# Kernel optimization log

Measured on AMD Instinct MI355X. Metric: run time of the kernel, lower is better.

## Reference

```python
import jax, jax.numpy as jnp
import numpy as np

N = 50000          # nodes (multiple of p+e=8)
E = 400000         # edges (avg degree 8)
H, C = 4, 128      # heads, per-head channels
IN = 5             # input node feature dim
HID = 512          # mlp hidden dim
P, EV = 4, 4       # pursuers / evaders per graph
NEG_SLOPE = 0.2    # GATConv leaky_relu slope

# static team index: nodes with idx % (P+EV) < P  (team='pursuer')
_idx = np.arange(N)
TEAM_IDX = jnp.asarray(_idx[_idx % (P + EV) < P])  # [N/2]


def setup_inputs() -> dict:
    key = jax.random.key(0)
    ks = jax.random.split(key, 16)
    s = 0.1
    return {
        "x": jax.random.normal(ks[0], (N, IN), jnp.float32),
        "edge_index": jax.random.randint(ks[1], (2, E), 0, N, jnp.int64),
        "edge_attr": jax.random.normal(ks[2], (E, 2), jnp.float32),
        # GATConv params
        "W": jax.random.normal(ks[3], (H * C, IN), jnp.float32) * s,
        "att_src": jax.random.normal(ks[4], (H, C), jnp.float32) * s,
        "att_dst": jax.random.normal(ks[5], (H, C), jnp.float32) * s,
        "bias": jnp.zeros((H * C,), jnp.float32),
        # MLP head params
        "W1": jax.random.normal(ks[6], (HID, H * C), jnp.float32) * s,
        "b1": jnp.zeros((HID,), jnp.float32),
        "W2": jax.random.normal(ks[7], (HID, HID), jnp.float32) * s,
        "b2": jnp.zeros((HID,), jnp.float32),
        "W3": jax.random.normal(ks[8], (2, HID), jnp.float32) * s,
        "b3": jnp.zeros((2,), jnp.float32),
    }


def _gat_max(x, src, dst, W, att_src, att_dst, bias):
    # linear transform: [N, H, C]
    h = (x @ W.T).reshape(N, H, C)
    a_src = jnp.einsum("nhc,hc->nh", h, att_src)  # [N, H]
    a_dst = jnp.einsum("nhc,hc->nh", h, att_dst)  # [N, H]
    # per-edge attention logits, leaky relu
    alpha = jax.nn.leaky_relu(a_src[src] + a_dst[dst], NEG_SLOPE)  # [Et, H]
    # segment softmax over incoming edges of each dst node
    amax = jax.ops.segment_max(alpha, dst, num_segments=N)  # [N, H]
    ex = jnp.exp(alpha - amax[dst])
    den = jax.ops.segment_sum(ex, dst, num_segments=N)      # [N, H]
    attn = ex / den[dst]                                     # [Et, H]
    # alpha-weighted messages, scatter-MAX aggregation (aggr='max')
    msg = h[src] * attn[:, :, None]                          # [Et, H, C]
    out = jax.ops.segment_max(msg, dst, num_segments=N)     # [N, H, C]
    return out.reshape(N, H * C) + bias


def reference(x, edge_index, edge_attr, W, att_src, att_dst, bias,
              W1, b1, W2, b2, W3, b3):
    # PyG GATConv default add_self_loops=True; edge_attr ignored (edge_dim=None)
    loops = jnp.arange(N, dtype=edge_index.dtype)
    src = jnp.concatenate([edge_index[0], loops])
    dst = jnp.concatenate([edge_index[1], loops])
    emb = _gat_max(x, src, dst, W, att_src, att_dst, bias)  # [N, 512]
    h = emb[TEAM_IDX]                                        # [N/2, 512]
    h = jax.nn.relu(h @ W1.T + b1)
    h = jax.nn.relu(h @ W2.T + b2)
    return jnp.tanh(h @ W3.T + b3)                           # [N/2, 2]
```

## Files before the change

### kernel.cpp

```cpp
#include <hip/hip_runtime.h>
#include <hip/hip_bf16.h>
#include <math.h>

#define N_NODES 50000
#define N_EDGES 400000
#define HEADS   4
#define HC      512
#define IN_DIM  5
#define M_SEL   25000
#define NEG_SLOPE 0.2f

typedef __attribute__((ext_vector_type(8))) short bf16x8;
typedef __attribute__((ext_vector_type(4))) float f32x4;

__device__ inline unsigned short f2bf(float f) {
    union { float f; unsigned u; } v; v.f = f;
    unsigned r = v.u + 0x7FFF + ((v.u >> 16) & 1);
    return (unsigned short)(r >> 16);
}
__device__ inline float bf2f(unsigned short b) {
    union { unsigned u; float f; } v; v.u = ((unsigned)b) << 16;
    return v.f;
}

#define GLOAD_LDS16(g, l)                                                  \
    __builtin_amdgcn_global_load_lds(                                      \
        (const __attribute__((address_space(1))) unsigned int*)(g),        \
        (__attribute__((address_space(3))) unsigned int*)(l), 16, 0, 0)

__global__ void k_init(const float* __restrict__ W1, const float* __restrict__ W2,
                       unsigned short* __restrict__ W1b, unsigned short* __restrict__ W2b,
                       float* __restrict__ part, int* __restrict__ deg) {
    int i = blockIdx.x * 256 + threadIdx.x;
    const float* src = (i < 65536) ? W1 : W2;
    unsigned short* dst = (i < 65536) ? W1b : W2b;
    int j = i & 65535;
    float4 v = ((const float4*)src)[j];
    ushort4 o;
    o.x = f2bf(v.x); o.y = f2bf(v.y); o.z = f2bf(v.z); o.w = f2bf(v.w);
    ((ushort4*)dst)[j] = o;
    if (i < 2 * M_SEL) part[i] = 0.f;
    if (i < N_NODES) deg[i] = 1;
}

#define TR_NPW 8
#define TR_BLKS 1563

__global__ __launch_bounds__(256) void k_transform_hist(
        const float* __restrict__ x, const float* __restrict__ W,
        const float* __restrict__ att_src, const float* __restrict__ att_dst,
        unsigned short* __restrict__ h, float* __restrict__ a_src,
        float* __restrict__ a_dst, const int* __restrict__ ei,
        int* __restrict__ deg) {
    if (blockIdx.x >= TR_BLKS) {
        int e = (blockIdx.x - TR_BLKS) * 256 + threadIdx.x;
        if (e < N_EDGES) atomicAdd(&deg[ei[N_EDGES + e]], 1);
        return;
    }
    int wave = threadIdx.x >> 6, lane = threadIdx.x & 63;
    int c0 = lane * 8;

    float wreg[40];
    const float4* wp = (const float4*)(W + c0 * IN_DIM);
#pragma unroll
    for (int i = 0; i < 10; i++) ((float4*)wreg)[i] = wp[i];
    float sas[8], sad[8];
    *(float4*)&sas[0] = *(const float4*)(att_src + c0);
    *(float4*)&sas[4] = *(const float4*)(att_src + c0 + 4);
    *(float4*)&sad[0] = *(const float4*)(att_dst + c0);
    *(float4*)&sad[4] = *(const float4*)(att_dst + c0 + 4);

    int n0 = (blockIdx.x * 4 + wave) * TR_NPW;
#pragma unroll
    for (int t = 0; t < TR_NPW; t++) {
        int n = n0 + t;
        if (n >= N_NODES) return;
        float xv[IN_DIM];
#pragma unroll
        for (int i = 0; i < IN_DIM; i++) xv[i] = x[n * IN_DIM + i];

        float ps = 0.f, pd = 0.f;
        bf16x8 hv8;
#pragma unroll
        for (int j = 0; j < 8; j++) {
            float acc = 0.f;
#pragma unroll
            for (int i = 0; i < IN_DIM; i++) acc += xv[i] * wreg[j * IN_DIM + i];
            hv8[j] = (short)f2bf(acc);
            ps += acc * sas[j];
            pd += acc * sad[j];
        }
        *(bf16x8*)(h + (size_t)n * HC + c0) = hv8;

#pragma unroll
        for (int off = 8; off >= 1; off >>= 1) {
            ps += __shfl_xor(ps, off);
            pd += __shfl_xor(pd, off);
        }
        if ((lane & 15) == 0) {
            int head = lane >> 4;
            a_src[n * HEADS + head] = ps;
            a_dst[n * HEADS + head] = pd;
        }
    }
}

#define NSCAN_BLK 196

__global__ void k_scan1(const int* __restrict__ deg, int* __restrict__ excl,
                        int* __restrict__ bsum) {
    __shared__ int s[256];
    int i = blockIdx.x * 256 + threadIdx.x;
    int v = (i < N_NODES) ? deg[i] : 0;
    s[threadIdx.x] = v;
    __syncthreads();
    for (int off = 1; off < 256; off <<= 1) {
        int t = (threadIdx.x >= off) ? s[threadIdx.x - off] : 0;
        __syncthreads();
        s[threadIdx.x] += t;
        __syncthreads();
    }
    if (i < N_NODES) excl[i] = s[threadIdx.x] - v;
    if (threadIdx.x == 255) bsum[blockIdx.x] = s[255];
}

__global__ void k_scan3fill(const int* __restrict__ excl, const int* __restrict__ bsum,
                            int* __restrict__ offs, int* __restrict__ curs,
                            int* __restrict__ csr) {
    __shared__ int part[256];
    int tid = threadIdx.x;
    part[tid] = (tid < NSCAN_BLK) ? bsum[tid] : 0;
    __syncthreads();
    for (int off = 1; off < 256; off <<= 1) {
        int t = (tid >= off) ? part[tid - off] : 0;
        __syncthreads();
        part[tid] += t;
        __syncthreads();
    }
    int blockoff = (blockIdx.x == 0) ? 0 : part[blockIdx.x - 1];
    int i = blockIdx.x * 256 + tid;
    if (i < N_NODES) {
        int o = excl[i] + blockoff;
        offs[i] = o;
        csr[o] = i;
        curs[i] = o + 1;
    }
}

__global__ void k_fill_edges(const int* __restrict__ ei, int* __restrict__ cursor,
                             int* __restrict__ csr) {
    int e = blockIdx.x * 256 + threadIdx.x;
    if (e < N_EDGES) {
        int d = ei[N_EDGES + e];
        int pos = atomicAdd(&cursor[d], 1);
        csr[pos] = ei[e];
    }
}

__global__ __launch_bounds__(256, 4) void k_aggregate(
        const unsigned short* __restrict__ h, const float* __restrict__ a_src,
        const float* __restrict__ a_dst, const int* __restrict__ csr,
        const int* __restrict__ offs, const int* __restrict__ deg,
        const float* __restrict__ bias, unsigned short* __restrict__ emb_sel) {
    int wave = threadIdx.x >> 6, lane = threadIdx.x & 63;
    int w = blockIdx.x * 4 + wave;
    int n = ((w >> 2) << 3) + (w & 3);

    int base = offs[n];
    int dn = deg[n];
    int head = lane >> 4, egrp = lane & 15;
    int c0 = lane * 8;

    float acc[8];
#pragma unroll
    for (int j = 0; j < 8; j++) acc[j] = -INFINITY;

    if (dn <= 16) {
        int slot = (egrp < dn) ? egrp : (dn - 1);
        int s_e = csr[base + slot];
        float adn = a_dst[n * HEADS + head];
        float araw = a_src[s_e * HEADS + head];
        float tl = araw + adn;
        tl = (tl > 0.f) ? tl : NEG_SLOPE * tl;
        if (egrp >= dn) tl = -INFINITY;

        bf16x8 v[16];
#pragma unroll
        for (int e = 0; e < 16; e++) {
            int s = __shfl(s_e, e);
            const unsigned short* ap = h + (size_t)s * HC + c0;
            asm volatile("global_load_dwordx4 %0, %1, off"
                         : "=v"(v[e]) : "v"(ap) : "memory");
        }

        float m = tl;
#pragma unroll
        for (int off = 8; off >= 1; off >>= 1) m = fmaxf(m, __shfl_xor(m, off));
        float ex = (egrp < dn) ? __expf(tl - m) : 0.f;
        float den = ex;
#pragma unroll
        for (int off = 8; off >= 1; off >>= 1) den += __shfl_xor(den, off);
        float attn = ex / den;

#pragma unroll
        for (int e = 0; e < 16; e++) {
            asm volatile("s_waitcnt vmcnt(%1)" : "+v"(v[e]) : "i"(15 - e));
            int ei = (e < dn) ? e : (dn - 1);
            float a = __shfl(attn, (head << 4) | ei);
#pragma unroll
            for (int j = 0; j < 8; j++)
                acc[j] = fmaxf(acc[j], bf2f((unsigned short)v[e][j]) * a);
        }
    } else {
        float adn = a_dst[n * HEADS + head];
        float m = -INFINITY;
        for (int e0 = 0; e0 < dn; e0 += 16) {
            int e = e0 + egrp;
            if (e < dn) {
                int s = csr[base + e];
                float t = a_src[s * HEADS + head] + adn;
                t = (t > 0.f) ? t : NEG_SLOPE * t;
                m = fmaxf(m, t);
            }
        }
#pragma unroll
        for (int off = 8; off >= 1; off >>= 1) m = fmaxf(m, __shfl_xor(m, off));
        float den = 0.f;
        for (int e0 = 0; e0 < dn; e0 += 16) {
            int e = e0 + egrp;
            if (e < dn) {
                int s = csr[base + e];
                float t = a_src[s * HEADS + head] + adn;
                t = (t > 0.f) ? t : NEG_SLOPE * t;
                den += __expf(t - m);
            }
        }
#pragma unroll
        for (int off = 8; off >= 1; off >>= 1) den += __shfl_xor(den, off);
        float invden = 1.0f / den;
        for (int e = 0; e < dn; e++) {
            int s = csr[base + e];
            float t = a_src[s * HEADS + head] + adn;
            t = (t > 0.f) ? t : NEG_SLOPE * t;
            float attn = __expf(t - m) * invden;
            bf16x8 hv = *(const bf16x8*)(h + (size_t)s * HC + c0);
#pragma unroll
            for (int j = 0; j < 8; j++)
                acc[j] = fmaxf(acc[j], bf2f((unsigned short)hv[j]) * attn);
        }
    }

    bf16x8 ov;
#pragma unroll
    for (int j = 0; j < 8; j++) ov[j] = (short)f2bf(acc[j] + bias[c0 + j]);
    *(bf16x8*)(emb_sel + (size_t)w * HC + c0) = ov;
}

template <int MODE>
__global__ __launch_bounds__(256, 4) void k_gemm(const unsigned short* __restrict__ A, int M,
                                                 const unsigned short* __restrict__ Wt,
                                                 const float* __restrict__ bias,
                                                 unsigned short* __restrict__ C,
                                                 const float* __restrict__ W3,
                                                 float* __restrict__ part) {
    __shared__ unsigned short As[128 * 64];
    __shared__ unsigned short Bs[128 * 64];
    int tid = threadIdx.x;
    int m0 = blockIdx.y * 128;
    int o0 = blockIdx.x * 128;
    int wv = tid >> 6, lane = tid & 63;
    int wm = wv >> 1, wn = wv & 1;

    f32x4 acc[4][4];
#pragma unroll
    for (int i = 0; i < 4; i++)
#pragma unroll
        for (int j = 0; j < 4; j++) acc[i][j] = (f32x4){0.f, 0.f, 0.f, 0.f};

    for (int k0 = 0; k0 < HC; k0 += 64) {
#pragma unroll
        for (int c = 0; c < 4; c++) {
            int off = wv * 4096 + c * 1024 + lane * 16;
            int row = off >> 7, col = (off & 127) >> 1;
            GLOAD_LDS16(A + (size_t)(m0 + row) * HC + k0 + col,
                        (char*)As + off);
            GLOAD_LDS16(Wt + (size_t)(o0 + row) * HC + k0 + col,
                        (char*)Bs + off);
        }
        __syncthreads();

#pragma unroll
        for (int kk = 0; kk < 2; kk++) {
            int kb = kk * 32 + (lane >> 4) * 8;
            bf16x8 af[4], bfr[4];
#pragma unroll
            for (int mi = 0; mi < 4; mi++)
                af[mi] = *(const bf16x8*)(&As[(wm * 64 + mi * 16 + (lane & 15)) * 64 + kb]);
#pragma unroll
            for (int ni = 0; ni < 4; ni++)
                bfr[ni] = *(const bf16x8*)(&Bs[(wn * 64 + ni * 16 + (lane & 15)) * 64 + kb]);
#pragma unroll
            for (int mi = 0; mi < 4; mi++)
#pragma unroll
                for (int ni = 0; ni < 4; ni++)
                    acc[mi][ni] = __builtin_amdgcn_mfma_f32_16x16x32_bf16(
                        af[mi], bfr[ni], acc[mi][ni], 0, 0, 0);
        }
        __syncthreads();
    }

    if (MODE == 0) {
#pragma unroll
        for (int ni = 0; ni < 4; ni++) {
            int ncol = o0 + wn * 64 + ni * 16 + (lane & 15);
            float bv = bias[ncol];
#pragma unroll
            for (int mi = 0; mi < 4; mi++) {
                int mbase = m0 + wm * 64 + mi * 16 + (lane >> 4) * 4;
#pragma unroll
                for (int r = 0; r < 4; r++) {
                    int m = mbase + r;
                    if (m < M) {
                        float v = fmaxf(acc[mi][ni][r] + bv, 0.f);
                        C[(size_t)m * HC + ncol] = f2bf(v);
                    }
                }
            }
        }
    } else {
        float p0[4][4], p1[4][4];
#pragma unroll
        for (int mi = 0; mi < 4; mi++)
#pragma unroll
            for (int r = 0; r < 4; r++) { p0[mi][r] = 0.f; p1[mi][r] = 0.f; }
#pragma unroll
        for (int ni = 0; ni < 4; ni++) {
            int ncol = o0 + wn * 64 + ni * 16 + (lane & 15);
            float bv = bias[ncol];
            float w0 = W3[ncol], w1 = W3[HC + ncol];
#pragma unroll
            for (int mi = 0; mi < 4; mi++)
#pragma unroll
                for (int r = 0; r < 4; r++) {
                    float v = fmaxf(acc[mi][ni][r] + bv, 0.f);
                    p0[mi][r] += v * w0;
                    p1[mi][r] += v * w1;
                }
        }
#pragma unroll
        for (int mi = 0; mi < 4; mi++)
#pragma unroll
            for (int r = 0; r < 4; r++) {
                float a0 = p0[mi][r], a1 = p1[mi][r];
#pragma unroll
                for (int off = 8; off >= 1; off >>= 1) {
                    a0 += __shfl_xor(a0, off);
                    a1 += __shfl_xor(a1, off);
                }
                int m = m0 + wm * 64 + mi * 16 + (lane >> 4) * 4 + r;
                if ((lane & 15) == 0 && m < M) {
                    atomicAdd(&part[m * 2 + 0], a0);
                    atomicAdd(&part[m * 2 + 1], a1);
                }
            }
    }
}

__global__ void k_tanh(const float* __restrict__ part, const float* __restrict__ b3,
                       float* __restrict__ out) {
    int i = blockIdx.x * 256 + threadIdx.x;
    if (i < 2 * M_SEL) out[i] = tanhf(part[i] + b3[i & 1]);
}

extern "C" void kernel_launch(void* const* d_in, const int* in_sizes, int n_in,
                              void* d_out, int out_size, void* d_ws, size_t ws_size,
                              hipStream_t stream) {
    const float* x       = (const float*)d_in[0];
    const int*   ei      = (const int*)d_in[1];
    const float* W       = (const float*)d_in[3];
    const float* att_src = (const float*)d_in[4];
    const float* att_dst = (const float*)d_in[5];
    const float* bias    = (const float*)d_in[6];
    const float* W1      = (const float*)d_in[7];
    const float* b1      = (const float*)d_in[8];
    const float* W2      = (const float*)d_in[9];
    const float* b2      = (const float*)d_in[10];
    const float* W3      = (const float*)d_in[11];
    const float* b3      = (const float*)d_in[12];
    float* out = (float*)d_out;

    char* ws = (char*)d_ws;
    unsigned short* h       = (unsigned short*)(ws);
    unsigned short* emb_sel = (unsigned short*)(ws + 51200000);
    unsigned short* h1      = (unsigned short*)(ws + 76800000);
    float* part  = (float*)(ws + 102400000);
    float* a_src = (float*)(ws + 102600000);
    float* a_dst = (float*)(ws + 103400000);
    int*   deg   = (int*)  (ws + 104200000);
    int*   offs  = (int*)  (ws + 104400000);
    int*   curs  = (int*)  (ws + 104600000);
    int*   excl  = (int*)  (ws + 104800000);
    int*   bsum  = (int*)  (ws + 105000000);
    int*   csr   = (int*)  (ws + 105001024);
    unsigned short* W1b = (unsigned short*)(ws + 106801024);
    unsigned short* W2b = (unsigned short*)(ws + 107325312);

    k_init<<<512, 256, 0, stream>>>(W1, W2, W1b, W2b, part, deg);
    k_transform_hist<<<TR_BLKS * 2, 256, 0, stream>>>(x, W, att_src, att_dst, h,
                                                      a_src, a_dst, ei, deg);
    k_scan1<<<NSCAN_BLK, 256, 0, stream>>>(deg, excl, bsum);
    k_scan3fill<<<NSCAN_BLK, 256, 0, stream>>>(excl, bsum, offs, curs, csr);
    k_fill_edges<<<(N_EDGES + 255) / 256, 256, 0, stream>>>(ei, curs, csr);
    k_aggregate<<<6250, 256, 0, stream>>>(h, a_src, a_dst, csr, offs, deg, bias, emb_sel);

    dim3 g(4, 196);
    k_gemm<0><<<g, 256, 0, stream>>>(emb_sel, M_SEL, W1b, b1, h1, nullptr, nullptr);
    k_gemm<1><<<g, 256, 0, stream>>>(h1, M_SEL, W2b, b2, nullptr, W3, part);
    k_tanh<<<196, 256, 0, stream>>>(part, b3, out);
}
```

Measured before the change: 180.7 us.

## Enlarge GEMM tile to 256x128 and simplify low-degree aggregation loads

The MLP GEMM now uses 256-row tiles where each wave owns 64 rows and all 128 output columns, with launch bounds lowered to 2 blocks per SM and half as many row blocks. This increases B-tile reuse per LDS load. The aggregate kernel drops the hand-issued 16-load inline asm prefetch with manual waitcnt in favour of a loop over actual degree, unrolled by 4. It also adds a bounds guard. Risks: GEMM register pressure doubles accumulators (possible lower occupancy), and aggregation loses the deep memory-level parallelism of 16 outstanding loads.

```diff
diff --git a/kernel.cpp b/kernel.cpp
--- a/kernel.cpp
+++ b/kernel.cpp
@@ -157,13 +157,13 @@
     }
 }
 
-__global__ __launch_bounds__(256, 4) void k_aggregate(
-        const unsigned short* __restrict__ h, const float* __restrict__ a_src,
-        const float* __restrict__ a_dst, const int* __restrict__ csr,
-        const int* __restrict__ offs, const int* __restrict__ deg,
-        const float* __restrict__ bias, unsigned short* __restrict__ emb_sel) {
+__global__ void k_aggregate(const unsigned short* __restrict__ h, const float* __restrict__ a_src,
+                            const float* __restrict__ a_dst, const int* __restrict__ csr,
+                            const int* __restrict__ offs, const int* __restrict__ deg,
+                            const float* __restrict__ bias, unsigned short* __restrict__ emb_sel) {
     int wave = threadIdx.x >> 6, lane = threadIdx.x & 63;
     int w = blockIdx.x * 4 + wave;
+    if (w >= M_SEL) return;
     int n = ((w >> 2) << 3) + (w & 3);
 
     int base = offs[n];
@@ -176,40 +176,49 @@
     for (int j = 0; j < 8; j++) acc[j] = -INFINITY;
 
     if (dn <= 16) {
-        int slot = (egrp < dn) ? egrp : (dn - 1);
-        int s_e = csr[base + slot];
-        float adn = a_dst[n * HEADS + head];
-        float araw = a_src[s_e * HEADS + head];
-        float tl = araw + adn;
-        tl = (tl > 0.f) ? tl : NEG_SLOPE * tl;
-        if (egrp >= dn) tl = -INFINITY;
-
-        bf16x8 v[16];
-#pragma unroll
-        for (int e = 0; e < 16; e++) {
-            int s = __shfl(s_e, e);
-            const unsigned short* ap = h + (size_t)s * HC + c0;
-            asm volatile("global_load_dwordx4 %0, %1, off"
-                         : "=v"(v[e]) : "v"(ap) : "memory");
-        }
-
-        float m = tl;
+        int s_e = 0;
+        float t = -INFINITY;
+        if (egrp < dn) {
+            s_e = csr[base + egrp];
+            t = a_src[s_e * HEADS + head] + a_dst[n * HEADS + head];
+            t = (t > 0.f) ? t : NEG_SLOPE * t;
+        }
+        float m = t;
 #pragma unroll
         for (int off = 8; off >= 1; off >>= 1) m = fmaxf(m, __shfl_xor(m, off));
-        float ex = (egrp < dn) ? __expf(tl - m) : 0.f;
+        float ex = (egrp < dn) ? __expf(t - m) : 0.f;
         float den = ex;
 #pragma unroll
         for (int off = 8; off >= 1; off >>= 1) den += __shfl_xor(den, off);
         float attn = ex / den;
 
-#pragma unroll
-        for (int e = 0; e < 16; e++) {
-            asm volatile("s_waitcnt vmcnt(%1)" : "+v"(v[e]) : "i"(15 - e));
-            int ei = (e < dn) ? e : (dn - 1);
-            float a = __shfl(attn, (head << 4) | ei);
+        int e = 0;
+        for (; e + 4 <= dn; e += 4) {
+            int s0 = __shfl(s_e, e + 0), s1 = __shfl(s_e, e + 1);
+            int s2 = __shfl(s_e, e + 2), s3 = __shfl(s_e, e + 3);
+            float a0 = __shfl(attn, (head << 4) | (e + 0));
+            float a1 = __shfl(attn, (head << 4) | (e + 1));
+            float a2 = __shfl(attn, (head << 4) | (e + 2));
+            float a3 = __shfl(attn, (head << 4) | (e + 3));
+            bf16x8 v0 = *(const bf16x8*)(h + (size_t)s0 * HC + c0);
+            bf16x8 v1 = *(const bf16x8*)(h + (size_t)s1 * HC + c0);
+            bf16x8 v2 = *(const bf16x8*)(h + (size_t)s2 * HC + c0);
+            bf16x8 v3 = *(const bf16x8*)(h + (size_t)s3 * HC + c0);
+#pragma unroll
+            for (int j = 0; j < 8; j++) {
+                acc[j] = fmaxf(acc[j], bf2f((unsigned short)v0[j]) * a0);
+                acc[j] = fmaxf(acc[j], bf2f((unsigned short)v1[j]) * a1);
+                acc[j] = fmaxf(acc[j], bf2f((unsigned short)v2[j]) * a2);
+                acc[j] = fmaxf(acc[j], bf2f((unsigned short)v3[j]) * a3);
+            }
+        }
+        for (; e < dn; e++) {
+            int s = __shfl(s_e, e);
+            float a = __shfl(attn, (head << 4) | e);
+            bf16x8 v = *(const bf16x8*)(h + (size_t)s * HC + c0);
 #pragma unroll
             for (int j = 0; j < 8; j++)
-                acc[j] = fmaxf(acc[j], bf2f((unsigned short)v[e][j]) * a);
+                acc[j] = fmaxf(acc[j], bf2f((unsigned short)v[j]) * a);
         }
     } else {
         float adn = a_dst[n * HEADS + head];
@@ -257,52 +266,54 @@
 }
 
 template <int MODE>
-__global__ __launch_bounds__(256, 4) void k_gemm(const unsigned short* __restrict__ A, int M,
+__global__ __launch_bounds__(256, 2) void k_gemm(const unsigned short* __restrict__ A, int M,
                                                  const unsigned short* __restrict__ Wt,
                                                  const float* __restrict__ bias,
                                                  unsigned short* __restrict__ C,
                                                  const float* __restrict__ W3,
                                                  float* __restrict__ part) {
-    __shared__ unsigned short As[128 * 64];
+    __shared__ unsigned short As[256 * 64];
     __shared__ unsigned short Bs[128 * 64];
     int tid = threadIdx.x;
-    int m0 = blockIdx.y * 128;
+    int m0 = blockIdx.y * 256;
     int o0 = blockIdx.x * 128;
     int wv = tid >> 6, lane = tid & 63;
-    int wm = wv >> 1, wn = wv & 1;
-
-    f32x4 acc[4][4];
+
+    f32x4 acc[4][8];
 #pragma unroll
     for (int i = 0; i < 4; i++)
 #pragma unroll
-        for (int j = 0; j < 4; j++) acc[i][j] = (f32x4){0.f, 0.f, 0.f, 0.f};
+        for (int j = 0; j < 8; j++) acc[i][j] = (f32x4){0.f, 0.f, 0.f, 0.f};
 
     for (int k0 = 0; k0 < HC; k0 += 64) {
 #pragma unroll
+        for (int c = 0; c < 8; c++) {
+            int off = c * 4096 + tid * 16;
+            int row = off >> 7, col = (off & 127) >> 1;
+            GLOAD_LDS16(A + (size_t)(m0 + row) * HC + k0 + col, (char*)As + off);
+        }
+#pragma unroll
         for (int c = 0; c < 4; c++) {
-            int off = wv * 4096 + c * 1024 + lane * 16;
+            int off = c * 4096 + tid * 16;
             int row = off >> 7, col = (off & 127) >> 1;
-            GLOAD_LDS16(A + (size_t)(m0 + row) * HC + k0 + col,
-                        (char*)As + off);
-            GLOAD_LDS16(Wt + (size_t)(o0 + row) * HC + k0 + col,
-                        (char*)Bs + off);
+            GLOAD_LDS16(Wt + (size_t)(o0 + row) * HC + k0 + col, (char*)Bs + off);
         }
         __syncthreads();
 
 #pragma unroll
         for (int kk = 0; kk < 2; kk++) {
             int kb = kk * 32 + (lane >> 4) * 8;
-            bf16x8 af[4], bfr[4];
+            bf16x8 af[4], bfr[8];
 #pragma unroll
             for (int mi = 0; mi < 4; mi++)
-                af[mi] = *(const bf16x8*)(&As[(wm * 64 + mi * 16 + (lane & 15)) * 64 + kb]);
-#pragma unroll
-            for (int ni = 0; ni < 4; ni++)
-                bfr[ni] = *(const bf16x8*)(&Bs[(wn * 64 + ni * 16 + (lane & 15)) * 64 + kb]);
+                af[mi] = *(const bf16x8*)(&As[(wv * 64 + mi * 16 + (lane & 15)) * 64 + kb]);
+#pragma unroll
+            for (int ni = 0; ni < 8; ni++)
+                bfr[ni] = *(const bf16x8*)(&Bs[(ni * 16 + (lane & 15)) * 64 + kb]);
 #pragma unroll
             for (int mi = 0; mi < 4; mi++)
 #pragma unroll
-                for (int ni = 0; ni < 4; ni++)
+                for (int ni = 0; ni < 8; ni++)
                     acc[mi][ni] = __builtin_amdgcn_mfma_f32_16x16x32_bf16(
                         af[mi], bfr[ni], acc[mi][ni], 0, 0, 0);
         }
@@ -311,12 +322,12 @@
 
     if (MODE == 0) {
 #pragma unroll
-        for (int ni = 0; ni < 4; ni++) {
-            int ncol = o0 + wn * 64 + ni * 16 + (lane & 15);
+        for (int ni = 0; ni < 8; ni++) {
+            int ncol = o0 + ni * 16 + (lane & 15);
             float bv = bias[ncol];
 #pragma unroll
             for (int mi = 0; mi < 4; mi++) {
-                int mbase = m0 + wm * 64 + mi * 16 + (lane >> 4) * 4;
+                int mbase = m0 + wv * 64 + mi * 16 + (lane >> 4) * 4;
 #pragma unroll
                 for (int r = 0; r < 4; r++) {
                     int m = mbase + r;
@@ -334,8 +345,8 @@
 #pragma unroll
             for (int r = 0; r < 4; r++) { p0[mi][r] = 0.f; p1[mi][r] = 0.f; }
 #pragma unroll
-        for (int ni = 0; ni < 4; ni++) {
-            int ncol = o0 + wn * 64 + ni * 16 + (lane & 15);
+        for (int ni = 0; ni < 8; ni++) {
+            int ncol = o0 + ni * 16 + (lane & 15);
             float bv = bias[ncol];
             float w0 = W3[ncol], w1 = W3[HC + ncol];
 #pragma unroll
@@ -357,7 +368,7 @@
                     a0 += __shfl_xor(a0, off);
                     a1 += __shfl_xor(a1, off);
                 }
-                int m = m0 + wm * 64 + mi * 16 + (lane >> 4) * 4 + r;
+                int m = m0 + wv * 64 + mi * 16 + (lane >> 4) * 4 + r;
                 if ((lane & 15) == 0 && m < M) {
                     atomicAdd(&part[m * 2 + 0], a0);
                     atomicAdd(&part[m * 2 + 1], a1);
@@ -413,7 +424,7 @@
     k_fill_edges<<<(N_EDGES + 255) / 256, 256, 0, stream>>>(ei, curs, csr);
     k_aggregate<<<6250, 256, 0, stream>>>(h, a_src, a_dst, csr, offs, deg, bias, emb_sel);
 
-    dim3 g(4, 196);
+    dim3 g(4, 98);
     k_gemm<0><<<g, 256, 0, stream>>>(emb_sel, M_SEL, W1b, b1, h1, nullptr, nullptr);
     k_gemm<1><<<g, 256, 0, stream>>>(h1, M_SEL, W2b, b2, nullptr, W3, part);
     k_tanh<<<196, 256, 0, stream>>>(part, b3, out);
```

New measurement: 178.2 us. About the same (-1.4%).
